# Kernel optimization log

Hardware: AMD Instinct MI355X
Metric: run time of the kernel (lower is better)

Reference implementation:

```python
import jax, jax.numpy as jnp
import numpy as np

N, D, K_FRAC = 4096, 256, 0.5
EPS = 1e-5  # BatchNorm1d default eps


def setup_inputs() -> dict:
    key = jax.random.key(0)
    kg, kh, kw = jax.random.split(key, 3)
    # sparse binary adjacency with self-loops so all degrees > 0 (pow(D,-1) finite)
    g = (jax.random.uniform(kg, (N, N)) < 0.004).astype(jnp.float32)
    g = jnp.maximum(g, jnp.eye(N, dtype=jnp.float32))
    h = jax.random.normal(kh, (N, D), dtype=jnp.float32)
    return {
        "g": g,
        "h": h,
        "gamma": jnp.ones((D,), jnp.float32),
        "beta": jnp.zeros((D,), jnp.float32),
        "w_proj": jax.random.normal(kw, (D, 1), dtype=jnp.float32) / np.sqrt(D),
        "b_proj": jnp.zeros((1,), jnp.float32),
        "sigma1": jnp.array([0.2], jnp.float32),
    }


def reference(g, h, gamma, beta, w_proj, b_proj, sigma1):
    # BatchNorm1d in training mode: batch statistics over the node axis
    mu = h.mean(0)
    var = h.var(0)  # biased variance, as torch uses for normalization
    h = (h - mu) / jnp.sqrt(var + EPS) * gamma + beta

    deg = g.sum(1)                               # [N] == Z2
    agg = (g @ h) / deg[:, None]                 # diag(D^-1) @ (g @ h), no NxN diag materialized
    Z1 = jnp.abs(h - agg).sum(1)                 # [N]
    pl = jax.nn.sigmoid(Z1 + deg)
    Z3 = (agg @ w_proj + b_proj)[:, 0]           # proj(Z3).squeeze()
    pg = jax.nn.softmax(Z3)                      # 1-D softmax (dim 0)
    pt = jax.nn.sigmoid(pl + pg)
    pf = jax.nn.sigmoid((h @ w_proj + b_proj)[:, 0])
    scores = sigma1[0] * pt + (1.0 - sigma1[0]) * pf

    # top_k_graph
    k = max(2, int(K_FRAC * N))
    _, idx = jax.lax.top_k(scores, k)            # [k]
    h_att = scores[:, None] * h                  # score-weighted features
    un_g = (g != 0).astype(jnp.float32)
    two_hop = ((un_g @ un_g) != 0).astype(jnp.float32)  # binarized 2-hop adjacency
    a_hat = two_hop[idx, :]                      # [k, N] row gather
    new_h = a_hat @ h_att                        # [k, D]
    g_new = a_hat[:, idx]                        # [k, k] column gather
    # norm_g: torch broadcast divides COLUMN j by row-sum degrees[j]
    g_new = g_new / g_new.sum(1)
    return g_new, new_h, idx
```

## Files before the change

kernel.cpp:

```cpp
#include <hip/hip_runtime.h>
#include <math.h>

#define NN 4096
#define DD 256
#define KK 2048
#define NW 64

__device__ __forceinline__ int build_list(const unsigned long long* __restrict__ B, int r,
                                          int l, int* cols, int cap) {
    unsigned long long word = B[(size_t)r * NW + l];
    int pc = __popcll(word);
    int off = pc;
    for (int d = 1; d < 64; d <<= 1) {
        int n = __shfl_up(off, d);
        if (l >= d) off += n;
    }
    int total = __shfl(off, 63);
    int base = off - pc;
    while (word) {
        int b = (int)__ffsll(word) - 1;
        word &= word - 1;
        if (base < cap) cols[base] = l * 64 + b;
        ++base;
    }
    return total;
}

__global__ void k_pre(const float* __restrict__ h, const float* __restrict__ g,
                      double* __restrict__ psum, double* __restrict__ psq,
                      unsigned long long* __restrict__ B) {
    int blk = blockIdx.x;
    int t = threadIdx.x;
    if (blk < 64) {
        int d = t;
        int r0 = blk * 64;
        double s0=0,s1=0,s2=0,s3=0,q0=0,q1=0,q2=0,q3=0;
        for (int k = 0; k < 64; k += 4) {
            double x0 = (double)h[(size_t)(r0+k+0) * DD + d];
            double x1 = (double)h[(size_t)(r0+k+1) * DD + d];
            double x2 = (double)h[(size_t)(r0+k+2) * DD + d];
            double x3 = (double)h[(size_t)(r0+k+3) * DD + d];
            s0 += x0; q0 += x0*x0;
            s1 += x1; q1 += x1*x1;
            s2 += x2; q2 += x2*x2;
            s3 += x3; q3 += x3*x3;
        }
        psum[blk * DD + d] = (s0+s1)+(s2+s3);
        psq [blk * DD + d] = (q0+q1)+(q2+q3);
    } else {
        int i = blk - 64;
        int q = t >> 6, l = t & 63;
        const float* gr = g + (size_t)i * NN;
        unsigned long long word = 0ull;
        int lw = l & 15;
        #pragma unroll
        for (int wi = 0; wi < 16; ++wi) {
            float v = gr[(q * 16 + wi) * 64 + l];
            unsigned long long m = __ballot(v != 0.0f);
            if (wi == lw) word = m;
        }
        if (l < 16) B[(size_t)i * NW + q * 16 + l] = word;
    }
}

__global__ void k_stats_final(const double* __restrict__ psum, const double* __restrict__ psq,
                              double* __restrict__ mu, double* __restrict__ rstd) {
    __shared__ double rs[4][DD];
    __shared__ double rq[4][DD];
    int t = threadIdx.x;
    int d = t & (DD - 1);
    int q = t >> 8;
    double s0=0,s1=0,q0=0,q1=0;
    int b0 = q * 16;
    for (int k = 0; k < 16; k += 2) {
        s0 += psum[(b0+k)   * DD + d];
        s1 += psum[(b0+k+1) * DD + d];
        q0 += psq [(b0+k)   * DD + d];
        q1 += psq [(b0+k+1) * DD + d];
    }
    rs[q][d] = s0 + s1;
    rq[q][d] = q0 + q1;
    __syncthreads();
    if (q == 0) {
        double S  = (rs[0][d]+rs[1][d]) + (rs[2][d]+rs[3][d]);
        double Q  = (rq[0][d]+rq[1][d]) + (rq[2][d]+rq[3][d]);
        double m  = S / (double)NN;
        double var = Q / (double)NN - m * m;
        mu[d]   = m;
        rstd[d] = 1.0 / sqrt(var + 1e-5);
    }
}

__global__ void k_main(const float* __restrict__ h, const double* __restrict__ mu,
                       const double* __restrict__ rstd, const float* __restrict__ gamma,
                       const float* __restrict__ beta, const unsigned long long* __restrict__ Bm,
                       const float* __restrict__ w, const float* __restrict__ bp,
                       float* __restrict__ hn, double* __restrict__ zpf,
                       unsigned long long* __restrict__ T, double* __restrict__ Z1,
                       double* __restrict__ Z3, int* __restrict__ degi) {
    __shared__ int cols[4][136];
    int blk = blockIdx.x;
    int t = threadIdx.x;
    int wv = t >> 6, l = t & 63;
    int r = blk * 4 + wv;
    int cnt = build_list(Bm, r, l, cols[wv], 128);
    if (cnt > 128) cnt = 128;
    const float4* h4 = (const float4*)h;
    double s0=0,s1=0,s2=0,s3=0,u0=0,u1=0,u2=0,u3=0;
    unsigned long long a0 = 0ull, a1 = 0ull;
    int j = 0;
    for (; j + 1 < cnt; j += 2) {
        int c0 = cols[wv][j], c1 = cols[wv][j + 1];
        float4 v0 = h4[(size_t)c0 * 64 + l];
        float4 v1 = h4[(size_t)c1 * 64 + l];
        a0 |= Bm[(size_t)c0 * NW + l];
        a1 |= Bm[(size_t)c1 * NW + l];
        s0 += (double)v0.x; s1 += (double)v0.y; s2 += (double)v0.z; s3 += (double)v0.w;
        u0 += (double)v1.x; u1 += (double)v1.y; u2 += (double)v1.z; u3 += (double)v1.w;
    }
    if (j < cnt) {
        int c0 = cols[wv][j];
        float4 v0 = h4[(size_t)c0 * 64 + l];
        a0 |= Bm[(size_t)c0 * NW + l];
        s0 += (double)v0.x; s1 += (double)v0.y; s2 += (double)v0.z; s3 += (double)v0.w;
    }
    T[(size_t)r * NW + l] = a0 | a1;
    s0 += u0; s1 += u1; s2 += u2; s3 += u3;
    const double2* mu2 = (const double2*)mu;
    const double2* rs2 = (const double2*)rstd;
    const float4*  ga4 = (const float4*)gamma;
    const float4*  be4 = (const float4*)beta;
    const float4*  w4  = (const float4*)w;
    double2 mA = mu2[2*l], mB = mu2[2*l+1];
    double2 rA = rs2[2*l], rB = rs2[2*l+1];
    float4 ga = ga4[l], be = be4[l], wl = w4[l];
    double inv = 1.0 / (double)cnt;
    double g0 = (s0 * inv - mA.x) * rA.x * (double)ga.x + (double)be.x;
    double g1 = (s1 * inv - mA.y) * rA.y * (double)ga.y + (double)be.y;
    double g2 = (s2 * inv - mB.x) * rB.x * (double)ga.z + (double)be.z;
    double g3 = (s3 * inv - mB.y) * rB.y * (double)ga.w + (double)be.w;
    float4 hv = h4[(size_t)r * 64 + l];
    double h0 = ((double)hv.x - mA.x) * rA.x * (double)ga.x + (double)be.x;
    double h1 = ((double)hv.y - mA.y) * rA.y * (double)ga.y + (double)be.y;
    double h2 = ((double)hv.z - mB.x) * rB.x * (double)ga.z + (double)be.z;
    double h3 = ((double)hv.w - mB.y) * rB.y * (double)ga.w + (double)be.w;
    float4 o = { (float)h0, (float)h1, (float)h2, (float)h3 };
    ((float4*)hn)[(size_t)r * 64 + l] = o;
    double z1p = (fabs(h0 - g0) + fabs(h1 - g1)) + (fabs(h2 - g2) + fabs(h3 - g3));
    double z3p = (g0 * (double)wl.x + g1 * (double)wl.y)
               + (g2 * (double)wl.z + g3 * (double)wl.w);
    double zfp = (h0 * (double)wl.x + h1 * (double)wl.y)
               + (h2 * (double)wl.z + h3 * (double)wl.w);
    for (int off = 32; off > 0; off >>= 1) {
        z1p += __shfl_down(z1p, off);
        z3p += __shfl_down(z3p, off);
        zfp += __shfl_down(zfp, off);
    }
    if (l == 0) {
        Z1[r] = z1p;
        Z3[r] = z3p + (double)bp[0];
        zpf[r] = zfp + (double)bp[0];
        degi[r] = cnt;
    }
}

__global__ void k_scorekeys(const double* __restrict__ Z1, const double* __restrict__ Z3,
                            const double* __restrict__ zpf, const int* __restrict__ degi,
                            const float* __restrict__ sigma1, float* __restrict__ scores,
                            unsigned long long* __restrict__ keys) {
    __shared__ double red[256];
    int t = threadIdx.x;
    double mx = -1e300;
    for (int k = 0; k < 16; ++k) mx = fmax(mx, Z3[t + 256 * k]);
    red[t] = mx;
    __syncthreads();
    for (int s = 128; s > 0; s >>= 1) {
        if (t < s) red[t] = fmax(red[t], red[t + s]);
        __syncthreads();
    }
    double M = red[0];
    __syncthreads();
    double se = 0.0;
    for (int k = 0; k < 16; ++k) se += exp(Z3[t + 256 * k] - M);
    red[t] = se;
    __syncthreads();
    for (int s = 128; s > 0; s >>= 1) {
        if (t < s) red[t] += red[t + s];
        __syncthreads();
    }
    double sum = red[0];
    int i = blockIdx.x * 256 + t;
    double s1 = (double)sigma1[0];
    double pg = exp(Z3[i] - M) / sum;
    double pl = 1.0 / (1.0 + exp(-(Z1[i] + (double)degi[i])));
    double pt = 1.0 / (1.0 + exp(-(pl + pg)));
    double pf = 1.0 / (1.0 + exp(-zpf[i]));
    float sc = (float)(s1 * pt + (1.0 - s1) * pf);
    scores[i] = sc;
    unsigned int b2 = __float_as_uint(sc);
    unsigned int ka = (b2 & 0x80000000u) ? ~b2 : (b2 ^ 0x80000000u);
    keys[i] = ((unsigned long long)(~ka) << 32) | (unsigned int)i;
}

__global__ void k_rank(const unsigned long long* __restrict__ keys, int* __restrict__ idx_int,
                       float* __restrict__ out_idx) {
    __shared__ unsigned long long Kl[NN];
    int t = threadIdx.x;
    for (int i = t; i < NN; i += 256) Kl[i] = keys[i];
    __syncthreads();
    int il = t >> 4, sub = t & 15;
    int i = blockIdx.x * 16 + il;
    unsigned long long ki = Kl[i];
    int c0 = 0, c1 = 0, c2 = 0, c3 = 0;
    for (int jj = 0; jj < 256; jj += 4) {
        int j = sub + (jj << 4);
        c0 += (Kl[j]      < ki) ? 1 : 0;
        c1 += (Kl[j + 16] < ki) ? 1 : 0;
        c2 += (Kl[j + 32] < ki) ? 1 : 0;
        c3 += (Kl[j + 48] < ki) ? 1 : 0;
    }
    int cnt = (c0 + c1) + (c2 + c3);
    for (int off = 8; off > 0; off >>= 1) cnt += __shfl_down(cnt, off, 16);
    if (sub == 0 && cnt < KK) {
        idx_int[cnt] = i;
        out_idx[cnt] = (float)i;
    }
}

__global__ void k_mid(const unsigned long long* __restrict__ T, const int* __restrict__ idx_int,
                      const float* __restrict__ scores, const float* __restrict__ hn,
                      float* __restrict__ inv_rs, float* __restrict__ h_att) {
    int blk = blockIdx.x;
    int t = threadIdx.x;
    if (blk < 128) {
        __shared__ unsigned long long Sl[NW];
        if (t < NW) Sl[t] = 0ull;
        __syncthreads();
        for (int j = t; j < KK; j += 256) {
            int ii = idx_int[j];
            atomicOr(&Sl[ii >> 6], 1ull << (ii & 63));
        }
        __syncthreads();
        int wv = t >> 6, l = t & 63;
        unsigned long long sw = Sl[l];
        #pragma unroll
        for (int k = 0; k < 4; ++k) {
            int j = blk * 16 + wv * 4 + k;
            int r = idx_int[j];
            int c = (int)__popcll(T[(size_t)r * NW + l] & sw);
            for (int off = 32; off > 0; off >>= 1) c += __shfl_down(c, off);
            if (l == 0) inv_rs[j] = 1.0f / (float)c;
        }
    } else {
        int i = (blk - 128) * 256 + t;
        float sc = scores[i >> 6];
        float4 v = ((const float4*)hn)[i];
        float4 o = { sc * v.x, sc * v.y, sc * v.z, sc * v.w };
        ((float4*)h_att)[i] = o;
    }
}

__global__ void k_out(const unsigned long long* __restrict__ T, const int* __restrict__ idx_int,
                      const float* __restrict__ inv_rs, const float* __restrict__ ha,
                      float* __restrict__ out_gnew, float* __restrict__ out_newh) {
    __shared__ unsigned long long Tl[NW];
    __shared__ int cols[2048];
    __shared__ int s_cnt;
    __shared__ float4 red[4][64];
    int blk = blockIdx.x;
    int t = threadIdx.x;
    if (blk < KK) {
        int r = blk;
        if (t < NW) Tl[t] = T[(size_t)idx_int[r] * NW + t];
        __syncthreads();
        const int4*   idx4 = (const int4*)idx_int;
        const float4* irs4 = (const float4*)inv_rs;
        float4* out4 = (float4*)(out_gnew + (size_t)r * KK);
        for (int c4 = t; c4 < KK / 4; c4 += 256) {
            int4 jc = idx4[c4];
            float4 iv = irs4[c4];
            float4 o;
            o.x = ((Tl[jc.x >> 6] >> (jc.x & 63)) & 1ull) ? iv.x : 0.0f;
            o.y = ((Tl[jc.y >> 6] >> (jc.y & 63)) & 1ull) ? iv.y : 0.0f;
            o.z = ((Tl[jc.z >> 6] >> (jc.z & 63)) & 1ull) ? iv.z : 0.0f;
            o.w = ((Tl[jc.w >> 6] >> (jc.w & 63)) & 1ull) ? iv.w : 0.0f;
            out4[c4] = o;
        }
    } else {
        int r = blk - KK;
        int wv = t >> 6, l = t & 63;
        if (t < 64) {
            int total = build_list(T, idx_int[r], t, cols, 2048);
            if (t == 63) s_cnt = total;
        }
        __syncthreads();
        int cnt = s_cnt < 2048 ? s_cnt : 2048;
        const float4* ha4 = (const float4*)ha;
        float4 a0 = {0,0,0,0}, a1 = {0,0,0,0}, a2 = {0,0,0,0}, a3 = {0,0,0,0};
        int j = wv;
        for (; j + 12 < cnt; j += 16) {
            int c0 = cols[j], c1 = cols[j + 4], c2 = cols[j + 8], c3 = cols[j + 12];
            float4 v0 = ha4[(size_t)c0 * 64 + l];
            float4 v1 = ha4[(size_t)c1 * 64 + l];
            float4 v2 = ha4[(size_t)c2 * 64 + l];
            float4 v3 = ha4[(size_t)c3 * 64 + l];
            a0.x += v0.x; a0.y += v0.y; a0.z += v0.z; a0.w += v0.w;
            a1.x += v1.x; a1.y += v1.y; a1.z += v1.z; a1.w += v1.w;
            a2.x += v2.x; a2.y += v2.y; a2.z += v2.z; a2.w += v2.w;
            a3.x += v3.x; a3.y += v3.y; a3.z += v3.z; a3.w += v3.w;
        }
        for (; j < cnt; j += 4) {
            int c0 = cols[j];
            float4 v0 = ha4[(size_t)c0 * 64 + l];
            a0.x += v0.x; a0.y += v0.y; a0.z += v0.z; a0.w += v0.w;
        }
        float4 acc;
        acc.x = (a0.x + a1.x) + (a2.x + a3.x);
        acc.y = (a0.y + a1.y) + (a2.y + a3.y);
        acc.z = (a0.z + a1.z) + (a2.z + a3.z);
        acc.w = (a0.w + a1.w) + (a2.w + a3.w);
        red[wv][l] = acc;
        __syncthreads();
        if (t < 64) {
            float4 r0 = red[0][t], r1 = red[1][t], r2 = red[2][t], r3 = red[3][t];
            float4 o;
            o.x = (r0.x + r1.x) + (r2.x + r3.x);
            o.y = (r0.y + r1.y) + (r2.y + r3.y);
            o.z = (r0.z + r1.z) + (r2.z + r3.z);
            o.w = (r0.w + r1.w) + (r2.w + r3.w);
            ((float4*)(out_newh + (size_t)r * DD))[t] = o;
        }
    }
}

extern "C" void kernel_launch(void* const* d_in, const int* in_sizes, int n_in,
                              void* d_out, int out_size, void* d_ws, size_t ws_size,
                              hipStream_t stream) {
    const float* g      = (const float*)d_in[0];
    const float* h      = (const float*)d_in[1];
    const float* gamma  = (const float*)d_in[2];
    const float* beta   = (const float*)d_in[3];
    const float* w_proj = (const float*)d_in[4];
    const float* b_proj = (const float*)d_in[5];
    const float* sigma1 = (const float*)d_in[6];

    char* p = (char*)d_ws;
    auto alloc = [&](size_t bytes) -> void* {
        void* q = (void*)p;
        p += (bytes + 255) & ~(size_t)255;
        return q;
    };
    double* mu      = (double*)alloc(DD * 8);
    double* rstd    = (double*)alloc(DD * 8);
    double* psum    = (double*)alloc(64 * DD * 8);
    double* psq     = (double*)alloc(64 * DD * 8);
    double* zpf     = (double*)alloc(NN * 8);
    double* Z1      = (double*)alloc(NN * 8);
    double* Z3      = (double*)alloc(NN * 8);
    int*    degi    = (int*)alloc(NN * 4);
    float*  scores  = (float*)alloc(NN * 4);
    unsigned long long* keys = (unsigned long long*)alloc(NN * 8);
    int*    idx_int = (int*)alloc(KK * 4);
    float*  inv_rs  = (float*)alloc(KK * 4);
    unsigned long long* B = (unsigned long long*)alloc((size_t)NN * NW * 8);
    unsigned long long* T = (unsigned long long*)alloc((size_t)NN * NW * 8);
    float*  hn      = (float*)alloc((size_t)NN * DD * 4);
    float*  h_att   = (float*)alloc((size_t)NN * DD * 4);

    float* out_gnew = (float*)d_out;
    float* out_newh = out_gnew + (size_t)KK * KK;
    float* out_idx  = out_newh + (size_t)KK * DD;

    hipLaunchKernelGGL(k_pre,         dim3(64 + NN), dim3(256),  0, stream, h, g, psum, psq, B);
    hipLaunchKernelGGL(k_stats_final, dim3(1),       dim3(1024), 0, stream, psum, psq, mu, rstd);
    hipLaunchKernelGGL(k_main,        dim3(1024),    dim3(256),  0, stream, h, mu, rstd, gamma, beta, B, w_proj, b_proj, hn, zpf, T, Z1, Z3, degi);
    hipLaunchKernelGGL(k_scorekeys,   dim3(16),      dim3(256),  0, stream, Z1, Z3, zpf, degi, sigma1, scores, keys);
    hipLaunchKernelGGL(k_rank,        dim3(256),     dim3(256),  0, stream, keys, idx_int, out_idx);
    hipLaunchKernelGGL(k_mid,         dim3(128 + 1024), dim3(256), 0, stream, T, idx_int, scores, hn, inv_rs, h_att);
    hipLaunchKernelGGL(k_out,         dim3(2 * KK),  dim3(256),  0, stream, T, idx_int, inv_rs, h_att, out_gnew, out_newh);
}
```

Baseline: 171.9 us.

## Compute new_h with bf16 MFMA on dense two-hop bit tiles using hi/lo split

Replaces the per-row sparse gather-sum for new_h with a dense matmul on MFMA bf16 instructions. The 2-hop bitmask rows are expanded into 0/1 bf16 A fragments, and score-weighted features are stored transposed as split hi/lo bf16 pairs to keep near-fp32 accuracy. K is split four ways into partial buffers that k_out then sums. This trades irregular gather loads for dense tensor-core work over all 4096 columns, adding transposed scatter writes and extra partial-buffer traffic.

```diff
diff --git a/kernel.cpp b/kernel.cpp
--- a/kernel.cpp
+++ b/kernel.cpp
@@ -5,6 +5,12 @@
 #define DD 256
 #define KK 2048
 #define NW 64
+#define SK 4
+#define KC (NN / SK)
+#define KW (KC / 32)
+
+typedef float f32x4  __attribute__((ext_vector_type(4)));
+typedef short bf16x8 __attribute__((ext_vector_type(8)));
 
 __device__ __forceinline__ int build_list(const unsigned long long* __restrict__ B, int r,
                                           int l, int* cols, int cap) {
@@ -229,7 +235,8 @@
 
 __global__ void k_mid(const unsigned long long* __restrict__ T, const int* __restrict__ idx_int,
                       const float* __restrict__ scores, const float* __restrict__ hn,
-                      float* __restrict__ inv_rs, float* __restrict__ h_att) {
+                      float* __restrict__ inv_rs, unsigned short* __restrict__ haT_hi,
+                      unsigned short* __restrict__ haT_lo) {
     int blk = blockIdx.x;
     int t = threadIdx.x;
     if (blk < 128) {
@@ -252,21 +259,91 @@
             if (l == 0) inv_rs[j] = 1.0f / (float)c;
         }
     } else {
-        int i = (blk - 128) * 256 + t;
-        float sc = scores[i >> 6];
-        float4 v = ((const float4*)hn)[i];
-        float4 o = { sc * v.x, sc * v.y, sc * v.z, sc * v.w };
-        ((float4*)h_att)[i] = o;
+        int bb = blk - 128;
+        int ng = bb & 63, dq = bb >> 6;
+        int wv = t >> 6, l = t & 63;
+        int node = ng * 64 + l;
+        float sc = scores[node];
+        const float* hr = hn + (size_t)node * DD;
+        for (int d = dq * 64 + wv; d < (dq + 1) * 64; d += 4) {
+            float x = hr[d] * sc;
+            unsigned int xb = __float_as_uint(x);
+            unsigned int hb = xb & 0xFFFF0000u;
+            float lo = x - __uint_as_float(hb);
+            unsigned int lb = __float_as_uint(lo);
+            haT_hi[(size_t)d * NN + node] = (unsigned short)(hb >> 16);
+            haT_lo[(size_t)d * NN + node] = (unsigned short)(lb >> 16);
+        }
+    }
+}
+
+__global__ void __launch_bounds__(256, 1)
+k_nh(const unsigned long long* __restrict__ T, const int* __restrict__ idx_int,
+     const unsigned short* __restrict__ haT_hi, const unsigned short* __restrict__ haT_lo,
+     float* __restrict__ part) {
+    __shared__ int ids[128];
+    __shared__ unsigned int Ab[128][KW + 1];
+    int blk = blockIdx.x;
+    int rs = blk & 15, cb = (blk >> 4) & 3, kc = blk >> 6;
+    int t = threadIdx.x;
+    if (t < 128) ids[t] = idx_int[rs * 128 + t];
+    __syncthreads();
+    for (int i = t; i < 128 * KW; i += 256) {
+        int row = i >> 5, w = i & (KW - 1);
+        Ab[row][w] = ((const unsigned int*)(T + (size_t)ids[row] * NW))[kc * KW + w];
+    }
+    __syncthreads();
+    int wv = t >> 6, l = t & 63;
+    int lm = l & 15, lg = l >> 4;
+    int row_base = (wv & 1) * 64;
+    int col_base = cb * 64 + (wv >> 1) * 32;
+    f32x4 acc[4][2];
+    #pragma unroll
+    for (int m = 0; m < 4; ++m) { acc[m][0] = (f32x4)0.0f; acc[m][1] = (f32x4)0.0f; }
+    const unsigned short* ph0 = haT_hi + (size_t)(col_base + lm) * NN + kc * KC + lg * 8;
+    const unsigned short* ph1 = ph0 + (size_t)16 * NN;
+    const unsigned short* pl0 = haT_lo + (size_t)(col_base + lm) * NN + kc * KC + lg * 8;
+    const unsigned short* pl1 = pl0 + (size_t)16 * NN;
+    #pragma unroll 2
+    for (int ks = 0; ks < KW; ++ks) {
+        bf16x8 bh0 = *(const bf16x8*)(ph0 + ks * 32);
+        bf16x8 bh1 = *(const bf16x8*)(ph1 + ks * 32);
+        bf16x8 bl0 = *(const bf16x8*)(pl0 + ks * 32);
+        bf16x8 bl1 = *(const bf16x8*)(pl1 + ks * 32);
+        #pragma unroll
+        for (int m = 0; m < 4; ++m) {
+            unsigned int bits = Ab[row_base + m * 16 + lm][ks];
+            unsigned int b8 = (bits >> (8 * lg)) & 0xFFu;
+            union { unsigned int u[4]; bf16x8 v; } au;
+            au.u[0] = ((b8 & 1u)        ? 0x3F80u : 0u) | ((b8 & 2u)   ? 0x3F800000u : 0u);
+            au.u[1] = (((b8 >> 2) & 1u) ? 0x3F80u : 0u) | ((b8 & 8u)   ? 0x3F800000u : 0u);
+            au.u[2] = (((b8 >> 4) & 1u) ? 0x3F80u : 0u) | ((b8 & 32u)  ? 0x3F800000u : 0u);
+            au.u[3] = (((b8 >> 6) & 1u) ? 0x3F80u : 0u) | ((b8 & 128u) ? 0x3F800000u : 0u);
+            bf16x8 a = au.v;
+            acc[m][0] = __builtin_amdgcn_mfma_f32_16x16x32_bf16(a, bh0, acc[m][0], 0, 0, 0);
+            acc[m][1] = __builtin_amdgcn_mfma_f32_16x16x32_bf16(a, bh1, acc[m][1], 0, 0, 0);
+            acc[m][0] = __builtin_amdgcn_mfma_f32_16x16x32_bf16(a, bl0, acc[m][0], 0, 0, 0);
+            acc[m][1] = __builtin_amdgcn_mfma_f32_16x16x32_bf16(a, bl1, acc[m][1], 0, 0, 0);
+        }
+    }
+    float* pp = part + (size_t)kc * ((size_t)KK * DD);
+    #pragma unroll
+    for (int m = 0; m < 4; ++m) {
+        int row0 = rs * 128 + row_base + m * 16 + lg * 4;
+        #pragma unroll
+        for (int n = 0; n < 2; ++n) {
+            int col = col_base + n * 16 + lm;
+            #pragma unroll
+            for (int r = 0; r < 4; ++r)
+                pp[(size_t)(row0 + r) * DD + col] = acc[m][n][r];
+        }
     }
 }
 
 __global__ void k_out(const unsigned long long* __restrict__ T, const int* __restrict__ idx_int,
-                      const float* __restrict__ inv_rs, const float* __restrict__ ha,
+                      const float* __restrict__ inv_rs, const float* __restrict__ part,
                       float* __restrict__ out_gnew, float* __restrict__ out_newh) {
     __shared__ unsigned long long Tl[NW];
-    __shared__ int cols[2048];
-    __shared__ int s_cnt;
-    __shared__ float4 red[4][64];
     int blk = blockIdx.x;
     int t = threadIdx.x;
     if (blk < KK) {
@@ -287,49 +364,18 @@
             out4[c4] = o;
         }
     } else {
-        int r = blk - KK;
-        int wv = t >> 6, l = t & 63;
-        if (t < 64) {
-            int total = build_list(T, idx_int[r], t, cols, 2048);
-            if (t == 63) s_cnt = total;
-        }
-        __syncthreads();
-        int cnt = s_cnt < 2048 ? s_cnt : 2048;
-        const float4* ha4 = (const float4*)ha;
-        float4 a0 = {0,0,0,0}, a1 = {0,0,0,0}, a2 = {0,0,0,0}, a3 = {0,0,0,0};
-        int j = wv;
-        for (; j + 12 < cnt; j += 16) {
-            int c0 = cols[j], c1 = cols[j + 4], c2 = cols[j + 8], c3 = cols[j + 12];
-            float4 v0 = ha4[(size_t)c0 * 64 + l];
-            float4 v1 = ha4[(size_t)c1 * 64 + l];
-            float4 v2 = ha4[(size_t)c2 * 64 + l];
-            float4 v3 = ha4[(size_t)c3 * 64 + l];
-            a0.x += v0.x; a0.y += v0.y; a0.z += v0.z; a0.w += v0.w;
-            a1.x += v1.x; a1.y += v1.y; a1.z += v1.z; a1.w += v1.w;
-            a2.x += v2.x; a2.y += v2.y; a2.z += v2.z; a2.w += v2.w;
-            a3.x += v3.x; a3.y += v3.y; a3.z += v3.z; a3.w += v3.w;
-        }
-        for (; j < cnt; j += 4) {
-            int c0 = cols[j];
-            float4 v0 = ha4[(size_t)c0 * 64 + l];
-            a0.x += v0.x; a0.y += v0.y; a0.z += v0.z; a0.w += v0.w;
-        }
-        float4 acc;
-        acc.x = (a0.x + a1.x) + (a2.x + a3.x);
-        acc.y = (a0.y + a1.y) + (a2.y + a3.y);
-        acc.z = (a0.z + a1.z) + (a2.z + a3.z);
-        acc.w = (a0.w + a1.w) + (a2.w + a3.w);
-        red[wv][l] = acc;
-        __syncthreads();
-        if (t < 64) {
-            float4 r0 = red[0][t], r1 = red[1][t], r2 = red[2][t], r3 = red[3][t];
-            float4 o;
-            o.x = (r0.x + r1.x) + (r2.x + r3.x);
-            o.y = (r0.y + r1.y) + (r2.y + r3.y);
-            o.z = (r0.z + r1.z) + (r2.z + r3.z);
-            o.w = (r0.w + r1.w) + (r2.w + r3.w);
-            ((float4*)(out_newh + (size_t)r * DD))[t] = o;
-        }
+        size_t off = (size_t)(blk - KK) * 1024 + (size_t)t * 4;
+        const size_t stride = (size_t)KK * DD;
+        float4 s0 = *(const float4*)(part + off);
+        float4 s1 = *(const float4*)(part + off + stride);
+        float4 s2 = *(const float4*)(part + off + 2 * stride);
+        float4 s3 = *(const float4*)(part + off + 3 * stride);
+        float4 o;
+        o.x = (s0.x + s1.x) + (s2.x + s3.x);
+        o.y = (s0.y + s1.y) + (s2.y + s3.y);
+        o.z = (s0.z + s1.z) + (s2.z + s3.z);
+        o.w = (s0.w + s1.w) + (s2.w + s3.w);
+        *(float4*)(out_newh + off) = o;
     }
 }
 
@@ -365,7 +411,9 @@
     unsigned long long* B = (unsigned long long*)alloc((size_t)NN * NW * 8);
     unsigned long long* T = (unsigned long long*)alloc((size_t)NN * NW * 8);
     float*  hn      = (float*)alloc((size_t)NN * DD * 4);
-    float*  h_att   = (float*)alloc((size_t)NN * DD * 4);
+    unsigned short* haT_hi = (unsigned short*)alloc((size_t)DD * NN * 2);
+    unsigned short* haT_lo = (unsigned short*)alloc((size_t)DD * NN * 2);
+    float*  part    = (float*)alloc((size_t)SK * KK * DD * 4);
 
     float* out_gnew = (float*)d_out;
     float* out_newh = out_gnew + (size_t)KK * KK;
@@ -376,6 +424,7 @@
     hipLaunchKernelGGL(k_main,        dim3(1024),    dim3(256),  0, stream, h, mu, rstd, gamma, beta, B, w_proj, b_proj, hn, zpf, T, Z1, Z3, degi);
     hipLaunchKernelGGL(k_scorekeys,   dim3(16),      dim3(256),  0, stream, Z1, Z3, zpf, degi, sigma1, scores, keys);
     hipLaunchKernelGGL(k_rank,        dim3(256),     dim3(256),  0, stream, keys, idx_int, out_idx);
-    hipLaunchKernelGGL(k_mid,         dim3(128 + 1024), dim3(256), 0, stream, T, idx_int, scores, hn, inv_rs, h_att);
-    hipLaunchKernelGGL(k_out,         dim3(2 * KK),  dim3(256),  0, stream, T, idx_int, inv_rs, h_att, out_gnew, out_newh);
-}
+    hipLaunchKernelGGL(k_mid,         dim3(128 + 256), dim3(256), 0, stream, T, idx_int, scores, hn, inv_rs, haT_hi, haT_lo);
+    hipLaunchKernelGGL(k_nh,          dim3(256),     dim3(256),  0, stream, T, idx_int, haT_hi, haT_lo, part);
+    hipLaunchKernelGGL(k_out,         dim3(KK + 512), dim3(256), 0, stream, T, idx_int, inv_rs, part, out_gnew, out_newh);
+}
```

Measured after the change: 171.0 us, median of 2. No clear change (-0.5%).
